# Kernel tuning notes

Hardware: AMD Instinct MI355X
Metric: run time of the kernel (lower is better)

The kernel has to match this reference:

```python
import jax, jax.numpy as jnp
import numpy as np

B, N2, N3, D = 16, 1024, 2048, 128


def setup_inputs() -> dict:
    key = jax.random.key(0)
    k1, k2 = jax.random.split(key)
    desc2d = jax.random.normal(k1, (B * N2, D), dtype=jnp.float32)
    desc3d = jax.random.normal(k2, (B * N3, D), dtype=jnp.float32)
    # uniform, sorted batch ids (equal-size segments -> jit-friendly ragged layout)
    idx2d = jnp.repeat(jnp.arange(B, dtype=jnp.int64), N2)
    idx3d = jnp.repeat(jnp.arange(B, dtype=jnp.int64), N3)
    return {"desc2d": desc2d, "idx2d": idx2d, "desc3d": desc3d, "idx3d": idx3d}


def reference(desc2d, idx2d, desc3d, idx3d):
    # number of batches from sorted batch ids (static, computed on host)
    nb = int(np.asarray(idx2d)[-1]) + 1
    n2 = desc2d.shape[0] // nb
    n3 = desc3d.shape[0] // nb
    d2 = desc2d.reshape(nb, n2, -1)  # [B, n2, D]
    d3 = desc3d.reshape(nb, n3, -1)  # [B, n3, D]
    d2 = d2 / jnp.linalg.norm(d2, axis=-1, keepdims=True)
    d3 = d3 / jnp.linalg.norm(d3, axis=-1, keepdims=True)
    sim = jnp.einsum('bid,bjd->bij', d3, d2)  # cosine similarity [B, n3, n2]
    # zero-pad one extra row and column per batch (dustbin), as in the original
    return jnp.pad(sim, ((0, 0), (0, 1), (0, 1)))
```

## Files before the change

### kernel.cpp

```cpp
#include <hip/hip_runtime.h>
#include <hip/hip_bf16.h>

#define NB   16
#define N2   1024
#define N3   2048
#define DD   128
#define OROWS (N3 + 1)
#define OCOLS (N2 + 1)

typedef __attribute__((ext_vector_type(8))) __bf16 bf16x8;
typedef __attribute__((ext_vector_type(4))) float  f32x4;

static __device__ __forceinline__ unsigned short f32_to_bf16(float f) {
    unsigned u = __float_as_uint(f);
    unsigned r = u + 0x7FFF + ((u >> 16) & 1);
    return (unsigned short)(r >> 16);
}

__global__ void normalize_kernel(const float* __restrict__ d2,
                                 const float* __restrict__ d3,
                                 unsigned short* __restrict__ ws) {
    const int row = blockIdx.x * 8 + (threadIdx.x >> 5);
    const int l   = threadIdx.x & 31;
    const float* src = (row < NB * N2)
        ? d2 + (size_t)row * DD
        : d3 + (size_t)(row - NB * N2) * DD;
    const float4 v = *reinterpret_cast<const float4*>(src + l * 4);
    float ss = v.x * v.x + v.y * v.y + v.z * v.z + v.w * v.w;
    #pragma unroll
    for (int off = 16; off; off >>= 1) ss += __shfl_xor(ss, off);
    const float s = rsqrtf(ss);
    ushort4 o;
    o.x = f32_to_bf16(v.x * s);
    o.y = f32_to_bf16(v.y * s);
    o.z = f32_to_bf16(v.z * s);
    o.w = f32_to_bf16(v.w * s);
    *reinterpret_cast<ushort4*>(ws + (size_t)row * DD + l * 4) = o;
}

__global__ __launch_bounds__(256, 2)
void gemm_kernel(const unsigned short* __restrict__ d3n,
                 const unsigned short* __restrict__ d2n,
                 float* __restrict__ out) {
    __shared__ char smem[65536];

    const int hw  = blockIdx.x;
    const int blk = (hw & 7) * 256 + (hw >> 3);

    const int b    = blk >> 7;
    const int tile = blk & 127;
    const int ti   = tile >> 3;
    const int tj   = tile & 7;

    const int t = threadIdx.x;

    const char* gA = (const char*)d3n + ((size_t)(b * N3 + ti * 128) << 8);
    const char* gB = (const char*)d2n + ((size_t)(b * N2 + tj * 128) << 8);

    #pragma unroll
    for (int it = 0; it < 8; ++it) {
        int o    = it * 4096 + t * 16;
        int row  = o >> 8;
        int colb = o & 255;
        int scol = colb ^ ((row & 7) << 4);
        __builtin_amdgcn_global_load_lds(
            (const __attribute__((address_space(1))) void*)(gA + row * 256 + scol),
            (__attribute__((address_space(3))) void*)(smem + o), 16, 0, 0);
    }
    #pragma unroll
    for (int it = 0; it < 8; ++it) {
        int o    = it * 4096 + t * 16;
        int row  = o >> 8;
        int colb = o & 255;
        int scol = colb ^ ((row & 7) << 4);
        __builtin_amdgcn_global_load_lds(
            (const __attribute__((address_space(1))) void*)(gB + row * 256 + scol),
            (__attribute__((address_space(3))) void*)(smem + 32768 + o), 16, 0, 0);
    }
    __syncthreads();

    const int wid = t >> 6;
    const int l   = t & 63;
    const int wm  = (wid >> 1) * 64;
    const int wn  = (wid & 1) * 64;
    const int lr  = l & 15;
    const int kq  = l >> 4;
    const int sw  = (lr & 7) << 4;

    f32x4 acc[4][4] = {};

    #pragma unroll
    for (int ks = 0; ks < 4; ++ks) {
        const int kb = ks * 64 + kq * 16;
        bf16x8 af[4], bfr[4];
        #pragma unroll
        for (int mi = 0; mi < 4; ++mi) {
            int r = wm + mi * 16 + lr;
            af[mi] = *reinterpret_cast<const bf16x8*>(smem + r * 256 + (kb ^ sw));
        }
        #pragma unroll
        for (int ni = 0; ni < 4; ++ni) {
            int r = wn + ni * 16 + lr;
            bfr[ni] = *reinterpret_cast<const bf16x8*>(smem + 32768 + r * 256 + (kb ^ sw));
        }
        #pragma unroll
        for (int mi = 0; mi < 4; ++mi)
            #pragma unroll
            for (int ni = 0; ni < 4; ++ni)
                acc[mi][ni] = __builtin_amdgcn_mfma_f32_16x16x32_bf16(
                    af[mi], bfr[ni], acc[mi][ni], 0, 0, 0);
    }

    float* obase = out + (size_t)b * OROWS * OCOLS
                       + (size_t)(ti * 128) * OCOLS + tj * 128;
    #pragma unroll
    for (int mi = 0; mi < 4; ++mi) {
        #pragma unroll
        for (int i = 0; i < 4; ++i) {
            int r = wm + mi * 16 + kq * 4 + i;
            #pragma unroll
            for (int ni = 0; ni < 4; ++ni) {
                int c = wn + ni * 16 + lr;
                obase[(size_t)r * OCOLS + c] = acc[mi][ni][i];
            }
        }
    }

    float* bb = out + (size_t)b * OROWS * OCOLS;
    if (tj == 7 && t < 128)
        bb[(size_t)(ti * 128 + t) * OCOLS + N2] = 0.0f;
    if (ti == 15) {
        if (t < 128)
            bb[(size_t)N3 * OCOLS + tj * 128 + t] = 0.0f;
        if (tj == 7 && t == 128)
            bb[(size_t)N3 * OCOLS + N2] = 0.0f;
    }
}

extern "C" void kernel_launch(void* const* d_in, const int* in_sizes, int n_in,
                              void* d_out, int out_size, void* d_ws, size_t ws_size,
                              hipStream_t stream) {
    (void)in_sizes; (void)n_in; (void)out_size; (void)ws_size;
    const float* desc2d = (const float*)d_in[0];
    const float* desc3d = (const float*)d_in[2];

    unsigned short* d2n = (unsigned short*)d_ws;
    unsigned short* d3n = d2n + (size_t)NB * N2 * DD;
    float* out = (float*)d_out;

    normalize_kernel<<<(NB * (N2 + N3)) / 8, 256, 0, stream>>>(desc2d, desc3d, d2n);
    gemm_kernel<<<NB * (N3 / 128) * (N2 / 128), 256, 0, stream>>>(d3n, d2n, out);
}
```

Baseline: 42.29 us.

## Stream B tiles per row-block with register-resident A and double buffering

```diff
diff --git a/kernel.cpp b/kernel.cpp
--- a/kernel.cpp
+++ b/kernel.cpp
@@ -38,102 +38,114 @@
     *reinterpret_cast<ushort4*>(ws + (size_t)row * DD + l * 4) = o;
 }
 
-__global__ __launch_bounds__(256, 2)
+__global__ __launch_bounds__(512, 1)
 void gemm_kernel(const unsigned short* __restrict__ d3n,
                  const unsigned short* __restrict__ d2n,
                  float* __restrict__ out) {
-    __shared__ char smem[65536];
+    __shared__ __align__(16) char smem[65536];
 
     const int hw  = blockIdx.x;
-    const int blk = (hw & 7) * 256 + (hw >> 3);
-
-    const int b    = blk >> 7;
-    const int tile = blk & 127;
-    const int ti   = tile >> 3;
-    const int tj   = tile & 7;
+    const int blk = (hw & 7) * 32 + (hw >> 3);
+    const int b   = blk >> 4;
+    const int ti  = blk & 15;
 
     const int t = threadIdx.x;
 
     const char* gA = (const char*)d3n + ((size_t)(b * N3 + ti * 128) << 8);
-    const char* gB = (const char*)d2n + ((size_t)(b * N2 + tj * 128) << 8);
+    const char* gB = (const char*)d2n + ((size_t)(b * N2) << 8);
 
     #pragma unroll
-    for (int it = 0; it < 8; ++it) {
-        int o    = it * 4096 + t * 16;
+    for (int it = 0; it < 4; ++it) {
+        int o    = it * 8192 + t * 16;
         int row  = o >> 8;
-        int colb = o & 255;
-        int scol = colb ^ ((row & 7) << 4);
+        int scol = (o & 255) ^ ((row & 7) << 4);
         __builtin_amdgcn_global_load_lds(
             (const __attribute__((address_space(1))) void*)(gA + row * 256 + scol),
             (__attribute__((address_space(3))) void*)(smem + o), 16, 0, 0);
     }
     #pragma unroll
-    for (int it = 0; it < 8; ++it) {
-        int o    = it * 4096 + t * 16;
+    for (int it = 0; it < 2; ++it) {
+        int o    = it * 8192 + t * 16;
         int row  = o >> 8;
-        int colb = o & 255;
-        int scol = colb ^ ((row & 7) << 4);
+        int scol = (o & 255) ^ ((row & 7) << 4);
         __builtin_amdgcn_global_load_lds(
             (const __attribute__((address_space(1))) void*)(gB + row * 256 + scol),
             (__attribute__((address_space(3))) void*)(smem + 32768 + o), 16, 0, 0);
     }
-    __syncthreads();
+    asm volatile("s_waitcnt vmcnt(0)" ::: "memory");
+    __builtin_amdgcn_s_barrier();
+    __builtin_amdgcn_sched_barrier(0);
 
     const int wid = t >> 6;
     const int l   = t & 63;
-    const int wm  = (wid >> 1) * 64;
-    const int wn  = (wid & 1) * 64;
+    const int wm  = (wid >> 2) * 64;
+    const int wn  = (wid & 3) * 16;
     const int lr  = l & 15;
     const int kq  = l >> 4;
     const int sw  = (lr & 7) << 4;
 
-    f32x4 acc[4][4] = {};
-
+    bf16x8 af[4][4];
     #pragma unroll
     for (int ks = 0; ks < 4; ++ks) {
         const int kb = ks * 64 + kq * 16;
-        bf16x8 af[4], bfr[4];
         #pragma unroll
         for (int mi = 0; mi < 4; ++mi) {
             int r = wm + mi * 16 + lr;
-            af[mi] = *reinterpret_cast<const bf16x8*>(smem + r * 256 + (kb ^ sw));
-        }
-        #pragma unroll
-        for (int ni = 0; ni < 4; ++ni) {
-            int r = wn + ni * 16 + lr;
-            bfr[ni] = *reinterpret_cast<const bf16x8*>(smem + 32768 + r * 256 + (kb ^ sw));
-        }
-        #pragma unroll
-        for (int mi = 0; mi < 4; ++mi)
-            #pragma unroll
-            for (int ni = 0; ni < 4; ++ni)
-                acc[mi][ni] = __builtin_amdgcn_mfma_f32_16x16x32_bf16(
-                    af[mi], bfr[ni], acc[mi][ni], 0, 0, 0);
-    }
-
-    float* obase = out + (size_t)b * OROWS * OCOLS
-                       + (size_t)(ti * 128) * OCOLS + tj * 128;
-    #pragma unroll
-    for (int mi = 0; mi < 4; ++mi) {
-        #pragma unroll
-        for (int i = 0; i < 4; ++i) {
-            int r = wm + mi * 16 + kq * 4 + i;
-            #pragma unroll
-            for (int ni = 0; ni < 4; ++ni) {
-                int c = wn + ni * 16 + lr;
-                obase[(size_t)r * OCOLS + c] = acc[mi][ni][i];
-            }
+            af[ks][mi] = *reinterpret_cast<const bf16x8*>(smem + r * 256 + (kb ^ sw));
         }
     }
 
-    float* bb = out + (size_t)b * OROWS * OCOLS;
-    if (tj == 7 && t < 128)
-        bb[(size_t)(ti * 128 + t) * OCOLS + N2] = 0.0f;
+    float* obase = out + (size_t)b * OROWS * OCOLS + (size_t)(ti * 128) * OCOLS;
+
+    for (int nj = 0; nj < 16; ++nj) {
+        const char* bbuf = smem + 32768 + (nj & 1) * 16384;
+
+        f32x4 acc[4] = {};
+        #pragma unroll
+        for (int ks = 0; ks < 4; ++ks) {
+            const int kb = ks * 64 + kq * 16;
+            int r = wn + lr;
+            bf16x8 bfr = *reinterpret_cast<const bf16x8*>(bbuf + r * 256 + (kb ^ sw));
+            #pragma unroll
+            for (int mi = 0; mi < 4; ++mi)
+                acc[mi] = __builtin_amdgcn_mfma_f32_16x16x32_bf16(
+                    af[ks][mi], bfr, acc[mi], 0, 0, 0);
+        }
+
+        if (nj < 15) {
+            const char* gBn = gB + (size_t)(nj + 1) * 16384;
+            char* nbuf = smem + 32768 + ((nj + 1) & 1) * 16384;
+            #pragma unroll
+            for (int it = 0; it < 2; ++it) {
+                int o    = it * 8192 + t * 16;
+                int row  = o >> 8;
+                int scol = (o & 255) ^ ((row & 7) << 4);
+                __builtin_amdgcn_global_load_lds(
+                    (const __attribute__((address_space(1))) void*)(gBn + row * 256 + scol),
+                    (__attribute__((address_space(3))) void*)(smem + ((nbuf - smem) + o)), 16, 0, 0);
+            }
+        }
+
+        #pragma unroll
+        for (int mi = 0; mi < 4; ++mi) {
+            #pragma unroll
+            for (int i = 0; i < 4; ++i) {
+                int r = wm + mi * 16 + kq * 4 + i;
+                int c = nj * 64 + wn + lr;
+                obase[(size_t)r * OCOLS + c] = acc[mi][i];
+            }
+        }
+
+        asm volatile("s_waitcnt vmcnt(16)" ::: "memory");
+        __builtin_amdgcn_s_barrier();
+        __builtin_amdgcn_sched_barrier(0);
+    }
+
+    if (t < 128)
+        obase[(size_t)t * OCOLS + N2] = 0.0f;
     if (ti == 15) {
-        if (t < 128)
-            bb[(size_t)N3 * OCOLS + tj * 128 + t] = 0.0f;
-        if (tj == 7 && t == 128)
-            bb[(size_t)N3 * OCOLS + N2] = 0.0f;
+        float* last = out + (size_t)b * OROWS * OCOLS + (size_t)N3 * OCOLS;
+        for (int c = t; c < OCOLS; c += 512) last[c] = 0.0f;
     }
 }
 
@@ -149,5 +161,5 @@
     float* out = (float*)d_out;
 
     normalize_kernel<<<(NB * (N2 + N3)) / 8, 256, 0, stream>>>(desc2d, desc3d, d2n);
-    gemm_kernel<<<NB * (N3 / 128) * (N2 / 128), 256, 0, stream>>>(d3n, d2n, out);
+    gemm_kernel<<<NB * (N3 / 128), 512, 0, stream>>>(d3n, d2n, out);
 }
```

Result: faster. 40.28 us (-4.8%).
